# Performance work log

Measured on AMD Instinct MI355X. Metric: run time of the kernel, lower is better.

The kernel has to match this reference:

```python
import jax, jax.numpy as jnp
import numpy as np

NDIM = 1024
NHEAD = 16
HEAD_DIM = NDIM // NHEAD


def setup_inputs() -> dict:
    key = jax.random.key(0)
    ks = jax.random.split(key, 12)
    B, L, C = 2, 2048, NDIM
    s = 0.02
    return {
        "q": jax.random.normal(ks[0], (B, L, C), jnp.float32),
        "k": jax.random.normal(ks[1], (B, L, C), jnp.float32),
        "v": jax.random.normal(ks[2], (B, L, C), jnp.float32),
        "Wq": jax.random.normal(ks[3], (C, C), jnp.float32) * s,
        "bq": jax.random.normal(ks[4], (C,), jnp.float32) * s,
        "Wk": jax.random.normal(ks[5], (C, C), jnp.float32) * s,
        "bk": jax.random.normal(ks[6], (C,), jnp.float32) * s,
        "Wv": jax.random.normal(ks[7], (C, C), jnp.float32) * s,
        "bv": jax.random.normal(ks[8], (C,), jnp.float32) * s,
        "Wo": jax.random.normal(ks[9], (C, C), jnp.float32) * s,
        "bo": jax.random.normal(ks[10], (C,), jnp.float32) * s,
    }


def reference(q, k, v, Wq, bq, Wk, bk, Wv, bv, Wo, bo):
    B, Lq, C = q.shape
    H, D = NHEAD, HEAD_DIM
    # projections, then split heads: (B, H, L, D)
    qh = (q @ Wq + bq).reshape(B, Lq, H, D).transpose(0, 2, 1, 3)
    kh = (k @ Wk + bk).reshape(B, k.shape[1], H, D).transpose(0, 2, 1, 3)
    vh = (v @ Wv + bv).reshape(B, v.shape[1], H, D).transpose(0, 2, 1, 3)
    scale = 1.0 / jnp.sqrt(jnp.asarray(D, qh.dtype))
    att = jnp.einsum("bhqd,bhkd->bhqk", qh, kh) * scale  # (B,H,Lq,Lk)
    att = jax.nn.softmax(att, axis=-1)  # dropout p=0.0 -> identity
    y = jnp.einsum("bhqk,bhkd->bhqd", att, vh)
    y = y.transpose(0, 2, 1, 3).reshape(B, Lq, C)
    return y @ Wo + bo
```

## Files before the change

kernel.cpp:

```cpp
#include <hip/hip_runtime.h>
#include <math.h>

#define BATCH 2
#define SEQ   2048
#define CDIM  1024
#define NHEAD 16
#define HDIM  64
#define TOKS  (BATCH * SEQ)

typedef __bf16 bf16x8 __attribute__((ext_vector_type(8)));
typedef __bf16 bf16x2 __attribute__((ext_vector_type(2)));
typedef float  f32x4  __attribute__((ext_vector_type(4)));

#define MFMA16(a, b, c) __builtin_amdgcn_mfma_f32_16x16x32_bf16(a, b, c, 0, 0, 0)

#define QSCALE 0.1803368801111204f

__device__ __forceinline__ void gload_lds16(const __bf16* g, __bf16* l) {
    __builtin_amdgcn_global_load_lds(
        (const __attribute__((address_space(1))) unsigned int*)g,
        (__attribute__((address_space(3))) unsigned int*)l, 16, 0, 0);
}

__global__ __launch_bounds__(256) void prep_kernel(
    const float* __restrict__ q, const float* __restrict__ k, const float* __restrict__ v,
    __bf16* __restrict__ qo, __bf16* __restrict__ ko, __bf16* __restrict__ vo,
    const float* __restrict__ W0, const float* __restrict__ W1,
    const float* __restrict__ W2, const float* __restrict__ W3,
    __bf16* __restrict__ T0, __bf16* __restrict__ T1,
    __bf16* __restrict__ T2, __bf16* __restrict__ T3)
{
    __shared__ __bf16 Ts[64][72];
    const int bx = blockIdx.x;
    const int tid = threadIdx.x;

    if (bx < 6144) {
        const int t = bx >> 11;
        const size_t i = ((size_t)(bx & 2047) * 256 + tid) * 8;
        const float* s = t == 0 ? q : (t == 1 ? k : v);
        __bf16* d = t == 0 ? qo : (t == 1 ? ko : vo);
        const float4 x = *(const float4*)&s[i];
        const float4 y = *(const float4*)&s[i + 4];
        bf16x8 o;
        o[0] = (__bf16)x.x; o[1] = (__bf16)x.y; o[2] = (__bf16)x.z; o[3] = (__bf16)x.w;
        o[4] = (__bf16)y.x; o[5] = (__bf16)y.y; o[6] = (__bf16)y.z; o[7] = (__bf16)y.w;
        *(bf16x8*)&d[i] = o;
        return;
    }

    const int t  = bx - 6144;
    const int z  = t >> 8;
    const int ry = (t & 255) >> 4;
    const int rx = t & 15;
    const float* W = z == 0 ? W0 : z == 1 ? W1 : z == 2 ? W2 : W3;
    __bf16* T = z == 0 ? T0 : z == 1 ? T1 : z == 2 ? T2 : T3;
    const int rb = ry * 64, cb = rx * 64;
    const int r = tid >> 4;
    const int c4 = (tid & 15) * 4;
#pragma unroll
    for (int p = 0; p < 4; p++) {
        const int rr = p * 16 + r;
        const float4 w4 = *(const float4*)&W[(size_t)(rb + rr) * CDIM + cb + c4];
        Ts[c4 + 0][rr] = (__bf16)w4.x;
        Ts[c4 + 1][rr] = (__bf16)w4.y;
        Ts[c4 + 2][rr] = (__bf16)w4.z;
        Ts[c4 + 3][rr] = (__bf16)w4.w;
    }
    __syncthreads();
    const int n = tid >> 2;
    const int k16 = (tid & 3) * 16;
    *(bf16x8*)&T[(size_t)(cb + n) * CDIM + rb + k16]     = *(const bf16x8*)&Ts[n][k16];
    *(bf16x8*)&T[(size_t)(cb + n) * CDIM + rb + k16 + 8] = *(const bf16x8*)&Ts[n][k16 + 8];
}

__global__ __launch_bounds__(256) void qkv_gemm_kernel(
    const __bf16* __restrict__ qb, const __bf16* __restrict__ kb,
    const __bf16* __restrict__ vb,
    const __bf16* __restrict__ Wqt, const __bf16* __restrict__ Wkt,
    const __bf16* __restrict__ Wvt,
    const float* __restrict__ bq, const float* __restrict__ bk,
    const float* __restrict__ bv,
    __bf16* __restrict__ Qh, __bf16* __restrict__ Kh, __bf16* __restrict__ Vht)
{
    __shared__ __bf16 As[128 * 32];
    __shared__ __bf16 Bs[128 * 32];

    const int z = blockIdx.z;
    const __bf16* A    = z == 0 ? qb : z == 1 ? kb : Wvt;
    const __bf16* Bt   = z == 0 ? Wqt : z == 1 ? Wkt : vb;
    const float*  bias = z == 0 ? bq : z == 1 ? bk : bv;

    const int tid  = threadIdx.x;
    const int w    = tid >> 6;
    const int lane = tid & 63;
    const int quad = lane >> 4;
    const int c    = lane & 15;
    const int wm   = w >> 1;
    const int wn   = w & 1;
    const int rowBase = (z == 2 ? blockIdx.x : blockIdx.y) * 128;
    const int colBase = (z == 2 ? blockIdx.y : blockIdx.x) * 128;

    const int sr = lane >> 2;
    const int sk = (lane & 3) * 8;

    f32x4 acc[4][4];
#pragma unroll
    for (int i = 0; i < 4; i++)
#pragma unroll
        for (int j = 0; j < 4; j++) acc[i][j] = (f32x4){0, 0, 0, 0};

    for (int k0 = 0; k0 < CDIM; k0 += 32) {
#pragma unroll
        for (int j = 0; j < 2; j++) {
            const int r0 = (w * 2 + j) * 16;
            gload_lds16(A  + (size_t)(rowBase + r0 + sr) * CDIM + k0 + sk, &As[r0 * 32]);
            gload_lds16(Bt + (size_t)(colBase + r0 + sr) * CDIM + k0 + sk, &Bs[r0 * 32]);
        }
        __syncthreads();

        bf16x8 af[4], bf[4];
#pragma unroll
        for (int i = 0; i < 4; i++) {
            af[i] = *(const bf16x8*)&As[(wm * 64 + i * 16 + c) * 32 + quad * 8];
            bf[i] = *(const bf16x8*)&Bs[(wn * 64 + i * 16 + c) * 32 + quad * 8];
        }
#pragma unroll
        for (int mi = 0; mi < 4; mi++)
#pragma unroll
            for (int ni = 0; ni < 4; ni++)
                acc[mi][ni] = MFMA16(af[mi], bf[ni], acc[mi][ni]);
        __syncthreads();
    }

#pragma unroll
    for (int mi = 0; mi < 4; mi++) {
#pragma unroll
        for (int ni = 0; ni < 4; ni++) {
            const int col = colBase + wn * 64 + ni * 16 + c;
#pragma unroll
            for (int r = 0; r < 4; r++) {
                const int row = rowBase + wm * 64 + mi * 16 + quad * 4 + r;
                const float val = acc[mi][ni][r];
                if (z == 2) {
                    const int col2 = (col & ~31) | (((col & 15) << 1) | ((col >> 4) & 1));
                    Vht[(size_t)row * TOKS + col2] = (__bf16)(val + bias[row]);
                } else {
                    const int b = row >> 11, l = row & 2047;
                    const int h = col >> 6,  d = col & 63;
                    const float s = (z == 0) ? QSCALE : 1.0f;
                    __bf16* outp = (z == 0) ? Qh : Kh;
                    outp[((((size_t)b * NHEAD + h) * SEQ) + l) * HDIM + d] =
                        (__bf16)((val + bias[col]) * s);
                }
            }
        }
    }
}

__global__ __launch_bounds__(256) void out_gemm_kernel(
    const __bf16* __restrict__ A, const __bf16* __restrict__ Bt,
    const float* __restrict__ bias, float* __restrict__ out)
{
    __shared__ __bf16 As[128 * 32];
    __shared__ __bf16 Bs[64 * 32];

    const int tid  = threadIdx.x;
    const int w    = tid >> 6;
    const int lane = tid & 63;
    const int quad = lane >> 4;
    const int c    = lane & 15;
    const int wm   = w >> 1;
    const int wn   = w & 1;
    const int rowBase = blockIdx.y * 128;
    const int colBase = blockIdx.x * 64;
    const int sr = lane >> 2;
    const int sk = (lane & 3) * 8;

    f32x4 acc[4][2];
#pragma unroll
    for (int i = 0; i < 4; i++)
#pragma unroll
        for (int j = 0; j < 2; j++) acc[i][j] = (f32x4){0, 0, 0, 0};

    for (int k0 = 0; k0 < CDIM; k0 += 32) {
#pragma unroll
        for (int j = 0; j < 2; j++) {
            const int r0 = (w * 2 + j) * 16;
            gload_lds16(A + (size_t)(rowBase + r0 + sr) * CDIM + k0 + sk, &As[r0 * 32]);
        }
        gload_lds16(Bt + (size_t)(colBase + w * 16 + sr) * CDIM + k0 + sk, &Bs[w * 16 * 32]);
        __syncthreads();

        bf16x8 af[4], bf[2];
#pragma unroll
        for (int i = 0; i < 4; i++)
            af[i] = *(const bf16x8*)&As[(wm * 64 + i * 16 + c) * 32 + quad * 8];
#pragma unroll
        for (int i = 0; i < 2; i++)
            bf[i] = *(const bf16x8*)&Bs[(wn * 32 + i * 16 + c) * 32 + quad * 8];
#pragma unroll
        for (int mi = 0; mi < 4; mi++)
#pragma unroll
            for (int ni = 0; ni < 2; ni++)
                acc[mi][ni] = MFMA16(af[mi], bf[ni], acc[mi][ni]);
        __syncthreads();
    }

#pragma unroll
    for (int mi = 0; mi < 4; mi++) {
#pragma unroll
        for (int ni = 0; ni < 2; ni++) {
            const int col = colBase + wn * 32 + ni * 16 + c;
#pragma unroll
            for (int r = 0; r < 4; r++) {
                const int row = rowBase + wm * 64 + mi * 16 + quad * 4 + r;
                out[(size_t)row * CDIM + col] = acc[mi][ni][r] + bias[col];
            }
        }
    }
}

__global__ __launch_bounds__(256) void attn_v5_kernel(
    const __bf16* __restrict__ Qh, const __bf16* __restrict__ Kh,
    const __bf16* __restrict__ Vht, __bf16* __restrict__ Y)
{
    __shared__ __align__(16) __bf16 Ks[2][32][72];
    __shared__ __align__(16) __bf16 Vt[2][64][48];
    __shared__ __align__(16) unsigned int Pf[4][2][16][36];

    const int tid  = threadIdx.x;
    const int w    = tid >> 6;
    const int lane = tid & 63;
    const int quad = lane >> 4;
    const int c    = lane & 15;
    const int bh   = blockIdx.x;
    const int b    = bh >> 4;
    const int h    = bh & 15;
    const int qbase = blockIdx.y * 128 + w * 32;

    const __bf16* Qg = Qh + (size_t)bh * SEQ * HDIM;
    const __bf16* Kg = Kh + (size_t)bh * SEQ * HDIM;
    const __bf16* Vg = Vht + (size_t)(h * HDIM) * TOKS + (size_t)b * SEQ;

    bf16x8 qf[2][2];
#pragma unroll
    for (int g = 0; g < 2; g++) {
        qf[g][0] = *(const bf16x8*)&Qg[(size_t)(qbase + g * 16 + c) * HDIM + quad * 8];
        qf[g][1] = *(const bf16x8*)&Qg[(size_t)(qbase + g * 16 + c) * HDIM + 32 + quad * 8];
    }

    bf16x8 ones;
#pragma unroll
    for (int j = 0; j < 8; j++) ones[j] = (__bf16)1.0f;

    f32x4 O[2][4];
    f32x4 L[2];
#pragma unroll
    for (int g = 0; g < 2; g++) {
        L[g] = (f32x4){0, 0, 0, 0};
#pragma unroll
        for (int i = 0; i < 4; i++) O[g][i] = (f32x4){0, 0, 0, 0};
    }

    const int krow = tid >> 3, kcol = (tid & 7) * 8;
    const int vrow = tid >> 2, vcol = (tid & 3) * 8;

    {
        const bf16x8 k0 = *(const bf16x8*)&Kg[(size_t)krow * HDIM + kcol];
        const bf16x8 v0 = *(const bf16x8*)&Vg[(size_t)vrow * TOKS + vcol];
        *(bf16x8*)&Ks[0][krow][kcol] = k0;
        *(bf16x8*)&Vt[0][vrow][vcol] = v0;
    }
    __syncthreads();

    int buf = 0;
    for (int t0 = 0; t0 < SEQ; t0 += 32) {
        const int tn = t0 + 32;
        bf16x8 kpre, vpre;
        if (tn < SEQ) {
            kpre = *(const bf16x8*)&Kg[(size_t)(tn + krow) * HDIM + kcol];
            vpre = *(const bf16x8*)&Vg[(size_t)vrow * TOKS + tn + vcol];
        }

        const bf16x8 k00 = *(const bf16x8*)&Ks[buf][c][quad * 8];
        const bf16x8 k01 = *(const bf16x8*)&Ks[buf][c][32 + quad * 8];
        const bf16x8 k10 = *(const bf16x8*)&Ks[buf][16 + c][quad * 8];
        const bf16x8 k11 = *(const bf16x8*)&Ks[buf][16 + c][32 + quad * 8];
        const bf16x8 v0 = *(const bf16x8*)&Vt[buf][c][quad * 8];
        const bf16x8 v1 = *(const bf16x8*)&Vt[buf][16 + c][quad * 8];
        const bf16x8 v2 = *(const bf16x8*)&Vt[buf][32 + c][quad * 8];
        const bf16x8 v3 = *(const bf16x8*)&Vt[buf][48 + c][quad * 8];

#pragma unroll
        for (int g = 0; g < 2; g++) {
            f32x4 s0 = {0, 0, 0, 0}, s1 = {0, 0, 0, 0};
            s0 = MFMA16(qf[g][0], k00, s0);
            s0 = MFMA16(qf[g][1], k01, s0);
            s1 = MFMA16(qf[g][0], k10, s1);
            s1 = MFMA16(qf[g][1], k11, s1);
#pragma unroll
            for (int r = 0; r < 4; r++) {
                union { bf16x2 v; unsigned int u; } pk;
                pk.v[0] = (__bf16)__builtin_amdgcn_exp2f(s0[r]);
                pk.v[1] = (__bf16)__builtin_amdgcn_exp2f(s1[r]);
                Pf[w][g][quad * 4 + r][c] = pk.u;
            }
            const bf16x8 pf = *(const bf16x8*)&Pf[w][g][c][quad * 4];
            L[g]    = MFMA16(pf, ones, L[g]);
            O[g][0] = MFMA16(pf, v0, O[g][0]);
            O[g][1] = MFMA16(pf, v1, O[g][1]);
            O[g][2] = MFMA16(pf, v2, O[g][2]);
            O[g][3] = MFMA16(pf, v3, O[g][3]);
        }

        if (tn < SEQ) {
            *(bf16x8*)&Ks[buf ^ 1][krow][kcol] = kpre;
            *(bf16x8*)&Vt[buf ^ 1][vrow][vcol] = vpre;
        }
        __syncthreads();
        buf ^= 1;
    }

    __bf16* Yb = Y + (size_t)b * SEQ * CDIM;
#pragma unroll
    for (int g = 0; g < 2; g++) {
#pragma unroll
        for (int r = 0; r < 4; r++) {
            const float inv = 1.0f / L[g][r];
            const int l = qbase + g * 16 + quad * 4 + r;
            __bf16* yp = Yb + (size_t)l * CDIM + h * HDIM + c;
            yp[0]  = (__bf16)(O[g][0][r] * inv);
            yp[16] = (__bf16)(O[g][1][r] * inv);
            yp[32] = (__bf16)(O[g][2][r] * inv);
            yp[48] = (__bf16)(O[g][3][r] * inv);
        }
    }
}


extern "C" void kernel_launch(void* const* d_in, const int* in_sizes, int n_in,
                              void* d_out, int out_size, void* d_ws, size_t ws_size,
                              hipStream_t stream)
{
    const float* q  = (const float*)d_in[0];
    const float* k  = (const float*)d_in[1];
    const float* v  = (const float*)d_in[2];
    const float* Wq = (const float*)d_in[3];
    const float* bq = (const float*)d_in[4];
    const float* Wk = (const float*)d_in[5];
    const float* bk = (const float*)d_in[6];
    const float* Wv = (const float*)d_in[7];
    const float* bv = (const float*)d_in[8];
    const float* Wo = (const float*)d_in[9];
    const float* bo = (const float*)d_in[10];
    float* out = (float*)d_out;

    const size_t MAT = (size_t)TOKS * CDIM;
    const size_t WN  = (size_t)CDIM * CDIM;

    __bf16* p   = (__bf16*)d_ws;
    __bf16* qb  = p; p += MAT;
    __bf16* kb  = p; p += MAT;
    __bf16* vb  = p; p += MAT;
    __bf16* Wqt = p; p += WN;
    __bf16* Wkt = p; p += WN;
    __bf16* Wvt = p; p += WN;
    __bf16* Wot = p; p += WN;
    __bf16* Qh  = p; p += MAT;
    __bf16* Kh  = p; p += MAT;
    __bf16* Vht = p; p += MAT;
    __bf16* Yb  = qb;

    prep_kernel<<<dim3(7168), dim3(256), 0, stream>>>(
        q, k, v, qb, kb, vb, Wq, Wk, Wv, Wo, Wqt, Wkt, Wvt, Wot);

    qkv_gemm_kernel<<<dim3(8, 32, 3), dim3(256), 0, stream>>>(
        qb, kb, vb, Wqt, Wkt, Wvt, bq, bk, bv, Qh, Kh, Vht);

    attn_v5_kernel<<<dim3(BATCH * NHEAD, SEQ / 128), dim3(256), 0, stream>>>(Qh, Kh, Vht, Yb);

    out_gemm_kernel<<<dim3(16, 32), dim3(256), 0, stream>>>(Yb, Wot, bo, out);
}
```

Baseline: 234.2 us.

## Double-buffer LDS tiles in QKV and output GEMMs and swap grid order

```diff
diff --git a/kernel.cpp b/kernel.cpp
--- a/kernel.cpp
+++ b/kernel.cpp
@@ -82,8 +82,8 @@
     const float* __restrict__ bv,
     __bf16* __restrict__ Qh, __bf16* __restrict__ Kh, __bf16* __restrict__ Vht)
 {
-    __shared__ __bf16 As[128 * 32];
-    __shared__ __bf16 Bs[128 * 32];
+    __shared__ __bf16 As[2][128 * 32];
+    __shared__ __bf16 Bs[2][128 * 32];
 
     const int z = blockIdx.z;
     const __bf16* A    = z == 0 ? qb : z == 1 ? kb : Wvt;
@@ -97,8 +97,8 @@
     const int c    = lane & 15;
     const int wm   = w >> 1;
     const int wn   = w & 1;
-    const int rowBase = (z == 2 ? blockIdx.x : blockIdx.y) * 128;
-    const int colBase = (z == 2 ? blockIdx.y : blockIdx.x) * 128;
+    const int rowBase = (z == 2 ? blockIdx.y : blockIdx.x) * 128;
+    const int colBase = (z == 2 ? blockIdx.x : blockIdx.y) * 128;
 
     const int sr = lane >> 2;
     const int sk = (lane & 3) * 8;
@@ -109,27 +109,36 @@
 #pragma unroll
         for (int j = 0; j < 4; j++) acc[i][j] = (f32x4){0, 0, 0, 0};
 
-    for (int k0 = 0; k0 < CDIM; k0 += 32) {
+    auto issue = [&](int bi, int k0) {
 #pragma unroll
         for (int j = 0; j < 2; j++) {
             const int r0 = (w * 2 + j) * 16;
-            gload_lds16(A  + (size_t)(rowBase + r0 + sr) * CDIM + k0 + sk, &As[r0 * 32]);
-            gload_lds16(Bt + (size_t)(colBase + r0 + sr) * CDIM + k0 + sk, &Bs[r0 * 32]);
-        }
-        __syncthreads();
+            gload_lds16(A  + (size_t)(rowBase + r0 + sr) * CDIM + k0 + sk, &As[bi][r0 * 32]);
+            gload_lds16(Bt + (size_t)(colBase + r0 + sr) * CDIM + k0 + sk, &Bs[bi][r0 * 32]);
+        }
+    };
+
+    issue(0, 0);
+    __syncthreads();
+
+    int buf = 0;
+    for (int k0 = 0; k0 < CDIM; k0 += 32) {
+        if (k0 + 32 < CDIM) issue(buf ^ 1, k0 + 32);
 
         bf16x8 af[4], bf[4];
 #pragma unroll
         for (int i = 0; i < 4; i++) {
-            af[i] = *(const bf16x8*)&As[(wm * 64 + i * 16 + c) * 32 + quad * 8];
-            bf[i] = *(const bf16x8*)&Bs[(wn * 64 + i * 16 + c) * 32 + quad * 8];
+            af[i] = *(const bf16x8*)&As[buf][(wm * 64 + i * 16 + c) * 32 + quad * 8];
+            bf[i] = *(const bf16x8*)&Bs[buf][(wn * 64 + i * 16 + c) * 32 + quad * 8];
         }
 #pragma unroll
         for (int mi = 0; mi < 4; mi++)
 #pragma unroll
             for (int ni = 0; ni < 4; ni++)
                 acc[mi][ni] = MFMA16(af[mi], bf[ni], acc[mi][ni]);
+
         __syncthreads();
+        buf ^= 1;
     }
 
 #pragma unroll
@@ -161,8 +170,8 @@
     const __bf16* __restrict__ A, const __bf16* __restrict__ Bt,
     const float* __restrict__ bias, float* __restrict__ out)
 {
-    __shared__ __bf16 As[128 * 32];
-    __shared__ __bf16 Bs[64 * 32];
+    __shared__ __bf16 As[2][128 * 32];
+    __shared__ __bf16 Bs[2][64 * 32];
 
     const int tid  = threadIdx.x;
     const int w    = tid >> 6;
@@ -171,8 +180,8 @@
     const int c    = lane & 15;
     const int wm   = w >> 1;
     const int wn   = w & 1;
-    const int rowBase = blockIdx.y * 128;
-    const int colBase = blockIdx.x * 64;
+    const int rowBase = blockIdx.x * 128;
+    const int colBase = blockIdx.y * 64;
     const int sr = lane >> 2;
     const int sk = (lane & 3) * 8;
 
@@ -182,28 +191,37 @@
 #pragma unroll
         for (int j = 0; j < 2; j++) acc[i][j] = (f32x4){0, 0, 0, 0};
 
-    for (int k0 = 0; k0 < CDIM; k0 += 32) {
+    auto issue = [&](int bi, int k0) {
 #pragma unroll
         for (int j = 0; j < 2; j++) {
             const int r0 = (w * 2 + j) * 16;
-            gload_lds16(A + (size_t)(rowBase + r0 + sr) * CDIM + k0 + sk, &As[r0 * 32]);
-        }
-        gload_lds16(Bt + (size_t)(colBase + w * 16 + sr) * CDIM + k0 + sk, &Bs[w * 16 * 32]);
-        __syncthreads();
+            gload_lds16(A + (size_t)(rowBase + r0 + sr) * CDIM + k0 + sk, &As[bi][r0 * 32]);
+        }
+        gload_lds16(Bt + (size_t)(colBase + w * 16 + sr) * CDIM + k0 + sk, &Bs[bi][w * 16 * 32]);
+    };
+
+    issue(0, 0);
+    __syncthreads();
+
+    int buf = 0;
+    for (int k0 = 0; k0 < CDIM; k0 += 32) {
+        if (k0 + 32 < CDIM) issue(buf ^ 1, k0 + 32);
 
         bf16x8 af[4], bf[2];
 #pragma unroll
         for (int i = 0; i < 4; i++)
-            af[i] = *(const bf16x8*)&As[(wm * 64 + i * 16 + c) * 32 + quad * 8];
+            af[i] = *(const bf16x8*)&As[buf][(wm * 64 + i * 16 + c) * 32 + quad * 8];
 #pragma unroll
         for (int i = 0; i < 2; i++)
-            bf[i] = *(const bf16x8*)&Bs[(wn * 32 + i * 16 + c) * 32 + quad * 8];
+            bf[i] = *(const bf16x8*)&Bs[buf][(wn * 32 + i * 16 + c) * 32 + quad * 8];
 #pragma unroll
         for (int mi = 0; mi < 4; mi++)
 #pragma unroll
             for (int ni = 0; ni < 2; ni++)
                 acc[mi][ni] = MFMA16(af[mi], bf[ni], acc[mi][ni]);
+
         __syncthreads();
+        buf ^= 1;
     }
 
 #pragma unroll
@@ -374,10 +392,10 @@
     prep_kernel<<<dim3(7168), dim3(256), 0, stream>>>(
         q, k, v, qb, kb, vb, Wq, Wk, Wv, Wo, Wqt, Wkt, Wvt, Wot);
 
-    qkv_gemm_kernel<<<dim3(8, 32, 3), dim3(256), 0, stream>>>(
+    qkv_gemm_kernel<<<dim3(32, 8, 3), dim3(256), 0, stream>>>(
         qb, kb, vb, Wqt, Wkt, Wvt, bq, bk, bv, Qh, Kh, Vht);
 
     attn_v5_kernel<<<dim3(BATCH * NHEAD, SEQ / 128), dim3(256), 0, stream>>>(Qh, Kh, Vht, Yb);
 
-    out_gemm_kernel<<<dim3(16, 32), dim3(256), 0, stream>>>(Yb, Wot, bo, out);
-}
+    out_gemm_kernel<<<dim3(32, 16), dim3(256), 0, stream>>>(Yb, Wot, bo, out);
+}
```

Measured after the change: 237.9 us. No clear change (+1.6%).
